# Optimization experiments

Measured on AMD Instinct MI355X. Metric: run time of the kernel, lower is better.

The kernel has to match this reference:

```python
import jax, jax.numpy as jnp
import numpy as np

EPS = 1e-06
LOG_BIAS = 1.0  # config.fire_log_bias


def setup_inputs() -> dict:
    key = jax.random.key(0)
    ks = jax.random.split(key, 5)
    S, H, W = 2048, 12, 32
    x = jax.random.normal(ks[0], (1, S, 768), dtype=jnp.float32)
    w1 = jax.random.normal(ks[1], (W, 1), dtype=jnp.float32) * 0.5
    b1 = jax.random.normal(ks[2], (W,), dtype=jnp.float32) * 0.1
    w2 = jax.random.normal(ks[3], (H, W), dtype=jnp.float32) * 0.2
    b2 = jax.random.normal(ks[4], (H,), dtype=jnp.float32) * 0.1
    c = jnp.float32(0.1)            # fire_init_c, trainable
    L_multiplier = jnp.float32(1.0)  # trainable
    init_L = jnp.float32(512.0)      # non-trainable buffer
    return {"x": x, "w1": w1, "b1": b1, "w2": w2, "b2": b2,
            "c": c, "L_multiplier": L_multiplier, "init_L": init_L}


def reference(x, w1, b1, w2, b2, c, L_multiplier, init_L):
    S = x.shape[1]
    pos = jnp.arange(S, dtype=jnp.float32)
    rel = pos[:, None] - pos[None, :]                      # [S, S]
    abs_rel = jnp.abs(rel) + EPS
    threshold = jnp.abs(L_multiplier * init_L)
    pos_norm = jnp.maximum(pos, threshold)[:, None] + EPS  # [S, 1]
    log_rel = jnp.log(abs_rel * c + LOG_BIAS + EPS)        # [S, S]
    log_norm = jnp.log(jnp.abs(c * pos_norm) + LOG_BIAS + EPS)  # [S, 1]
    nd = log_rel / log_norm                                # [S, S]
    # tiny MLP: Linear(1,W) -> ReLU -> Linear(W,H)
    h = jax.nn.relu(nd[..., None] * w1[:, 0] + b1)         # [S, S, W]
    bias = jnp.einsum('stw,hw->hst', h, w2) + b2[:, None, None]  # [H, S, S]
    return bias[None]                                      # [1, H, S, S]
```

## Files before the change

kernel.cpp:

```cpp
#include <hip/hip_runtime.h>
#include <math.h>


#define SDIM 2048
#define WDIM 32
#define HDIM 12
#define NK 33
#define EPSF 1e-6f
#define LOGB 1.0f

typedef float f32x4 __attribute__((ext_vector_type(4)));

__global__ __launch_bounds__(512) void fire_fused(
    const float* __restrict__ w1, const float* __restrict__ b1,
    const float* __restrict__ w2, const float* __restrict__ b2,
    const float* __restrict__ cptr, const float* __restrict__ lmptr,
    const float* __restrict__ ilptr, float* __restrict__ out)
{
    __shared__ __align__(16) float sLR[SDIM];
    __shared__ __align__(16) float sAB[NK * 24];
    __shared__ float sTp[64];
    __shared__ float traw[WDIM], w1s[WDIM], b1s[WDIM];
    __shared__ int   rnk[WDIM], neg[WDIM];
    __shared__ float sLn[2];

    const int tid = threadIdx.x;
    const int i   = blockIdx.x;
    const float c = cptr[0];

    {
        const int d0 = tid * 4;
        #pragma unroll
        for (int e = 0; e < 4; ++e) {
            const float d = (float)(d0 + e);
            sLR[d0 + e] = logf(fmaf(d + EPSF, c, LOGB + EPSF));
        }
    }
    if (tid == 0) {
        const float thr = fabsf(lmptr[0] * ilptr[0]);
        const float pn  = fmaxf((float)i, thr) + EPSF;
        const float ln  = logf(fabsf(c * pn) + LOGB + EPSF);
        sLn[0] = ln; sLn[1] = 1.0f / ln;
    }
    if (tid < WDIM) {
        const float a = w1[tid], b = b1[tid];
        w1s[tid] = a; b1s[tid] = b;
        float t; int isneg;
        if (a > 0.f)      { t = -b / a; isneg = 0; }
        else if (a < 0.f) { t = -b / a; isneg = 1; }
        else {
            t = (b > 0.f) ? -INFINITY : INFINITY; isneg = 0;
        }
        traw[tid] = t; neg[tid] = isneg;
    }
    __syncthreads();

    if (tid < WDIM) {
        const float t = traw[tid];
        int r = 0;
        for (int v = 0; v < WDIM; ++v) {
            const float tv = traw[v];
            if (tv < t || (tv == t && v < tid)) r++;
        }
        rnk[tid] = r;
        sTp[r] = t * sLn[0];
    } else if (tid < 64) {
        sTp[tid] = INFINITY;
    }
    __syncthreads();

    if (tid < NK * HDIM) {
        const int k = tid / HDIM;
        const int h = tid % HDIM;
        float a = 0.f, bb = 0.f;
        for (int w = 0; w < WDIM; ++w) {
            const bool active = neg[w] ? (rnk[w] >= k) : (rnk[w] < k);
            if (active) {
                const float w2v = w2[h * WDIM + w];
                a  += w2v * w1s[w];
                bb += w2v * b1s[w];
            }
        }
        bb += b2[h];
        sAB[k * 24 + h * 2 + 0] = a * sLn[1];
        sAB[k * 24 + h * 2 + 1] = bb;
    }
    __syncthreads();

    const int j0 = tid * 4;
    float lrv[4];
    int   kk[4];
    #pragma unroll
    for (int e = 0; e < 4; ++e) {
        const int j = j0 + e;
        int dd = i - j; if (dd < 0) dd = -dd;
        const float x = sLR[dd];
        int k = 0;
        if (x > sTp[k + 31]) k += 32;
        if (x > sTp[k + 15]) k += 16;
        if (x > sTp[k + 7])  k += 8;
        if (x > sTp[k + 3])  k += 4;
        if (x > sTp[k + 1])  k += 2;
        if (x > sTp[k])      k += 1;
        kk[e] = k;
        lrv[e] = x;
    }

    const size_t base = (size_t)i * SDIM + (size_t)j0;
    #pragma unroll
    for (int hp = 0; hp < 6; ++hp) {
        f32x4 va, vb;
        #pragma unroll
        for (int e = 0; e < 4; ++e) {
            const f32x4 ab = *(const f32x4*)&sAB[kk[e] * 24 + hp * 4];
            va[e] = fmaf(ab.x, lrv[e], ab.y);
            vb[e] = fmaf(ab.z, lrv[e], ab.w);
        }
        *(f32x4*)(out + (size_t)(2 * hp)     * SDIM * SDIM + base) = va;
        *(f32x4*)(out + (size_t)(2 * hp + 1) * SDIM * SDIM + base) = vb;
    }
}

extern "C" void kernel_launch(void* const* d_in, const int* in_sizes, int n_in,
                              void* d_out, int out_size, void* d_ws, size_t ws_size,
                              hipStream_t stream)
{
    const float* w1 = (const float*)d_in[1];
    const float* b1 = (const float*)d_in[2];
    const float* w2 = (const float*)d_in[3];
    const float* b2 = (const float*)d_in[4];
    const float* c  = (const float*)d_in[5];
    const float* lm = (const float*)d_in[6];
    const float* il = (const float*)d_in[7];
    float* out = (float*)d_out;

    fire_fused<<<SDIM, 512, 0, stream>>>(w1, b1, w2, b2, c, lm, il, out);
}
```

Baseline: 226.2 us.

## Process four output rows per block to amortize per-block table setup

Each block now handles four rows instead of one, so the log table, threshold ranking and per-segment coefficient setup are amortized over four rows. To make the tables row-independent, the per-row log-norm scaling moves from the thresholds and slopes onto the input value (x = log_rel / log_norm), and the reciprocal log-norm is computed per row. Grid size drops to a quarter, which reduces parallelism (512 blocks) but cuts redundant setup work and syncs.

```diff
diff --git a/kernel.cpp b/kernel.cpp
--- a/kernel.cpp
+++ b/kernel.cpp
@@ -6,6 +6,7 @@
 #define WDIM 32
 #define HDIM 12
 #define NK 33
+#define NROWS 4
 #define EPSF 1e-6f
 #define LOGB 1.0f
 
@@ -19,13 +20,11 @@
 {
     __shared__ __align__(16) float sLR[SDIM];
     __shared__ __align__(16) float sAB[NK * 24];
-    __shared__ float sTp[64];
+    __shared__ float sT[64];
     __shared__ float traw[WDIM], w1s[WDIM], b1s[WDIM];
     __shared__ int   rnk[WDIM], neg[WDIM];
-    __shared__ float sLn[2];
 
     const int tid = threadIdx.x;
-    const int i   = blockIdx.x;
     const float c = cptr[0];
 
     {
@@ -35,12 +34,6 @@
             const float d = (float)(d0 + e);
             sLR[d0 + e] = logf(fmaf(d + EPSF, c, LOGB + EPSF));
         }
-    }
-    if (tid == 0) {
-        const float thr = fabsf(lmptr[0] * ilptr[0]);
-        const float pn  = fmaxf((float)i, thr) + EPSF;
-        const float ln  = logf(fabsf(c * pn) + LOGB + EPSF);
-        sLn[0] = ln; sLn[1] = 1.0f / ln;
     }
     if (tid < WDIM) {
         const float a = w1[tid], b = b1[tid];
@@ -63,9 +56,9 @@
             if (tv < t || (tv == t && v < tid)) r++;
         }
         rnk[tid] = r;
-        sTp[r] = t * sLn[0];
+        sT[r] = t;
     } else if (tid < 64) {
-        sTp[tid] = INFINITY;
+        sT[tid] = INFINITY;
     }
     __syncthreads();
 
@@ -82,42 +75,51 @@
             }
         }
         bb += b2[h];
-        sAB[k * 24 + h * 2 + 0] = a * sLn[1];
+        sAB[k * 24 + h * 2 + 0] = a;
         sAB[k * 24 + h * 2 + 1] = bb;
     }
     __syncthreads();
 
-    const int j0 = tid * 4;
-    float lrv[4];
-    int   kk[4];
-    #pragma unroll
-    for (int e = 0; e < 4; ++e) {
-        const int j = j0 + e;
-        int dd = i - j; if (dd < 0) dd = -dd;
-        const float x = sLR[dd];
-        int k = 0;
-        if (x > sTp[k + 31]) k += 32;
-        if (x > sTp[k + 15]) k += 16;
-        if (x > sTp[k + 7])  k += 8;
-        if (x > sTp[k + 3])  k += 4;
-        if (x > sTp[k + 1])  k += 2;
-        if (x > sTp[k])      k += 1;
-        kk[e] = k;
-        lrv[e] = x;
-    }
+    const float thr = fabsf(lmptr[0] * ilptr[0]);
+    const int   i0  = (int)blockIdx.x * NROWS;
+    const int   j0  = tid * 4;
 
-    const size_t base = (size_t)i * SDIM + (size_t)j0;
-    #pragma unroll
-    for (int hp = 0; hp < 6; ++hp) {
-        f32x4 va, vb;
+    for (int r = 0; r < NROWS; ++r) {
+        const int i = i0 + r;
+        const float pn  = fmaxf((float)i, thr) + EPSF;
+        const float ivl = 1.0f / logf(fabsf(c * pn) + LOGB + EPSF);
+
+        float ndv[4];
+        int   kk[4];
         #pragma unroll
         for (int e = 0; e < 4; ++e) {
-            const f32x4 ab = *(const f32x4*)&sAB[kk[e] * 24 + hp * 4];
-            va[e] = fmaf(ab.x, lrv[e], ab.y);
-            vb[e] = fmaf(ab.z, lrv[e], ab.w);
+            const int j = j0 + e;
+            int dd = i - j; if (dd < 0) dd = -dd;
+            const float x = sLR[dd] * ivl;
+            int k = 0;
+            if (x > sT[k + 31]) k += 32;
+            if (x > sT[k + 15]) k += 16;
+            if (x > sT[k + 7])  k += 8;
+            if (x > sT[k + 3])  k += 4;
+            if (x > sT[k + 1])  k += 2;
+            if (x > sT[k])      k += 1;
+            kk[e] = k;
+            ndv[e] = x;
         }
-        *(f32x4*)(out + (size_t)(2 * hp)     * SDIM * SDIM + base) = va;
-        *(f32x4*)(out + (size_t)(2 * hp + 1) * SDIM * SDIM + base) = vb;
+
+        const size_t base = (size_t)i * SDIM + (size_t)j0;
+        #pragma unroll
+        for (int hp = 0; hp < 6; ++hp) {
+            f32x4 va, vb;
+            #pragma unroll
+            for (int e = 0; e < 4; ++e) {
+                const f32x4 ab = *(const f32x4*)&sAB[kk[e] * 24 + hp * 4];
+                va[e] = fmaf(ab.x, ndv[e], ab.y);
+                vb[e] = fmaf(ab.z, ndv[e], ab.w);
+            }
+            *(f32x4*)(out + (size_t)(2 * hp)     * SDIM * SDIM + base) = va;
+            *(f32x4*)(out + (size_t)(2 * hp + 1) * SDIM * SDIM + base) = vb;
+        }
     }
 }
 
@@ -134,5 +136,5 @@
     const float* il = (const float*)d_in[7];
     float* out = (float*)d_out;
 
-    fire_fused<<<SDIM, 512, 0, stream>>>(w1, b1, w2, b2, c, lm, il, out);
+    fire_fused<<<SDIM / NROWS, 512, 0, stream>>>(w1, b1, w2, b2, c, lm, il, out);
 }
```

New measurement: 213.4 us. -5.7%, faster.
